# Kernel optimization log

Measured on AMD Instinct MI355X. Metric: run time of the kernel, lower is better.

The kernel has to match this reference:

```python
import jax, jax.numpy as jnp
import numpy as np

HIDDEN = 2048
QK_DIM = 2048
NUM_HEADS = 16
HEAD_DIM = QK_DIM // NUM_HEADS  # 128; RoPE rotates this many dims per head
B, T = 4, 2048
EPS = 1e-5


def setup_inputs() -> dict:
    key = jax.random.key(0)
    ks = jax.random.split(key, 10)
    return {
        "q_state": jax.random.normal(ks[0], (B, T, HIDDEN), jnp.float32),
        "k_state": jax.random.normal(ks[1], (B, T, HIDDEN), jnp.float32),
        "v_state": jax.random.normal(ks[2], (B, T, HIDDEN), jnp.float32),
        # torch Linear weights: [out_features, in_features], no bias
        "Wq": jax.random.normal(ks[3], (QK_DIM, HIDDEN), jnp.float32) * 0.02,
        "Wk": jax.random.normal(ks[4], (QK_DIM, HIDDEN), jnp.float32) * 0.02,
        "Wv": jax.random.normal(ks[5], (HIDDEN, HIDDEN), jnp.float32) * 0.02,
        "negator": jnp.asarray(1.0, jnp.float32),
        "q_gamma": jnp.ones((2 * QK_DIM,), jnp.float32),
        "q_beta": jnp.zeros((2 * QK_DIM,), jnp.float32),
        "k_gamma": jnp.ones((2 * QK_DIM,), jnp.float32),
        "k_beta": jnp.zeros((2 * QK_DIM,), jnp.float32),
        "offset": 0,
    }


def _layer_norm(x, gamma, beta):
    mu = jnp.mean(x, axis=-1, keepdims=True)
    var = jnp.mean(jnp.square(x - mu), axis=-1, keepdims=True)
    return (x - mu) * jax.lax.rsqrt(var + EPS) * gamma + beta


def _split_heads(x, n_heads):
    b, t, d = x.shape
    return x.reshape(b, t, n_heads, d // n_heads).transpose(0, 2, 1, 3)  # b h t f


def _rotate_half(x):
    # interleaved pairs: (x1, x2) -> (-x2, x1)
    x2 = x.reshape(*x.shape[:-1], x.shape[-1] // 2, 2)
    return jnp.stack((-x2[..., 1], x2[..., 0]), axis=-1).reshape(x.shape)


def _apply_rope(x, offset, rot_dim):
    # x: [b, h, t, f]; rotate first rot_dim features, pass the rest through
    t = (jnp.arange(x.shape[-2]) + offset).astype(jnp.float32)
    inv_freq = 1.0 / (10000.0 ** (jnp.arange(0, rot_dim, 2, dtype=jnp.float32) / rot_dim))
    freqs = t[:, None] * inv_freq[None, :]           # [t, rot_dim/2]
    freqs = jnp.repeat(freqs, 2, axis=-1)            # [t, rot_dim] interleaved
    cos, sin = jnp.cos(freqs), jnp.sin(freqs)
    xl, xr = x[..., :rot_dim], x[..., rot_dim:]
    xl = xl * cos + _rotate_half(xl) * sin
    return jnp.concatenate([xl, xr], axis=-1)


def reference(q_state, k_state, v_state, Wq, Wk, Wv, negator,
              q_gamma, q_beta, k_gamma, k_beta, offset):
    q = jnp.einsum("btd,fd->btf", q_state, Wq)
    k = jnp.einsum("btd,fd->btf", k_state, Wk)
    v = jnp.einsum("btd,fd->btf", v_state, Wv)
    q = jnp.concatenate((q, negator - q), axis=-1)   # [b, t, 2*QK_DIM]
    k = jnp.concatenate((k, negator - k), axis=-1)
    q = _layer_norm(q, q_gamma, q_beta)
    k = _layer_norm(k, k_gamma, k_beta)
    q = _split_heads(q, NUM_HEADS)                   # [b, h, t, 2*HEAD_DIM]
    k = _split_heads(k, NUM_HEADS)
    v = _split_heads(v, NUM_HEADS)                   # [b, h, t, HIDDEN/h]
    q = _apply_rope(q, offset, HEAD_DIM)
    k = _apply_rope(k, offset, HEAD_DIM)
    return q, k, v
```

## Files before the change

kernel.cpp:

```cpp
#include <hip/hip_runtime.h>
#include <hip/hip_fp16.h>

#define TDIM 2048
#define BDIM 4
#define MROWS 8192
#define NDIM 2048
#define KDIM 2048
#define NH 16

typedef __attribute__((ext_vector_type(8))) _Float16 f16x8;
typedef __attribute__((ext_vector_type(4))) _Float16 f16x4;
typedef __attribute__((ext_vector_type(4))) float f32x4;

__device__ __forceinline__ void load16_to_lds(const _Float16* g, _Float16* l) {
  __builtin_amdgcn_global_load_lds((const __attribute__((address_space(1))) void*)g,
                                   (__attribute__((address_space(3))) void*)l,
                                   16, 0, 0);
}

#define WAITBAR(N) do { \
  asm volatile("s_waitcnt vmcnt(" #N ")" ::: "memory"); \
  __builtin_amdgcn_s_barrier(); \
  __builtin_amdgcn_sched_barrier(0); \
} while (0)

__global__ __launch_bounds__(256) void cvt6_kernel(
    const float* __restrict__ s0, const float* __restrict__ s1,
    const float* __restrict__ s2, const float* __restrict__ s3,
    const float* __restrict__ s4, const float* __restrict__ s5,
    _Float16* __restrict__ d0, _Float16* __restrict__ d1,
    _Float16* __restrict__ d2, _Float16* __restrict__ d3,
    _Float16* __restrict__ d4, _Float16* __restrict__ d5) {
  const int z = blockIdx.z;
  const float* s; _Float16* d; int n;
  switch (z) {
    case 0: s = s0; d = d0; n = MROWS * KDIM; break;
    case 1: s = s1; d = d1; n = MROWS * KDIM; break;
    case 2: s = s2; d = d2; n = MROWS * KDIM; break;
    case 3: s = s3; d = d3; n = NDIM * KDIM; break;
    case 4: s = s4; d = d4; n = NDIM * KDIM; break;
    default: s = s5; d = d5; n = NDIM * KDIM; break;
  }
  const int n4 = n >> 2;
  const int stride = gridDim.x * blockDim.x;
  for (int i = blockIdx.x * blockDim.x + threadIdx.x; i < n4; i += stride) {
    float4 f = ((const float4*)s)[i];
    f16x4 h;
    h.x = (_Float16)f.x; h.y = (_Float16)f.y;
    h.z = (_Float16)f.z; h.w = (_Float16)f.w;
    ((f16x4*)d)[i] = h;
  }
}

__global__ __launch_bounds__(512, 2) void gemm_kernel(
    const _Float16* __restrict__ A0, const _Float16* __restrict__ A1,
    const _Float16* __restrict__ A2,
    const _Float16* __restrict__ W0, const _Float16* __restrict__ W1,
    const _Float16* __restrict__ W2,
    _Float16* __restrict__ qraw, _Float16* __restrict__ kraw,
    float* __restrict__ vout) {
  __shared__ __align__(16) _Float16 lds[4][2][8192];

  int lin = (blockIdx.z * gridDim.y + blockIdx.y) * gridDim.x + blockIdx.x;
  lin = (lin & 7) * 96 + (lin >> 3);
  const int z  = lin >> 8;
  const int ty = (lin >> 3) & 31;
  const int tx = lin & 7;

  const _Float16* __restrict__ A  = (z == 0) ? A0 : ((z == 1) ? A1 : A2);
  const _Float16* __restrict__ Wt = (z == 0) ? W0 : ((z == 1) ? W1 : W2);
  const int m0 = ty * 256;
  const int n0 = tx * 256;

  const int tid  = threadIdx.x;
  const int wave = tid >> 6;
  const int lane = tid & 63;
  const int m_in = lane & 15;
  const int kq   = lane >> 4;
  const int wave_m = wave >> 2;
  const int wave_n = wave & 3;

  f32x4 acc[8][4];
  const f32x4 z4 = {0.f, 0.f, 0.f, 0.f};
#pragma unroll
  for (int i = 0; i < 8; ++i)
#pragma unroll
    for (int j = 0; j < 4; ++j) acc[i][j] = z4;

  const int P0 = tid * 16;
  const int P1 = (512 + tid) * 16;
  const int L0 = P0 ^ (((P0 >> 7) & 3) << 4);
  const int L1 = P1 ^ (((P1 >> 7) & 3) << 4);
  const _Float16* srcA0 = A  + (size_t)(m0 + (L0 >> 6)) * KDIM + ((L0 & 63) >> 1);
  const _Float16* srcA1 = A  + (size_t)(m0 + (L1 >> 6)) * KDIM + ((L1 & 63) >> 1);
  const _Float16* srcB0 = Wt + (size_t)(n0 + (L0 >> 6)) * KDIM + ((L0 & 63) >> 1);
  const _Float16* srcB1 = Wt + (size_t)(n0 + (L1 >> 6)) * KDIM + ((L1 & 63) >> 1);
  const int dst0 = (wave * 64) * 8;
  const int dst1 = (512 + wave * 64) * 8;

  int offA[8], offB[4];
#pragma unroll
  for (int mi = 0; mi < 8; ++mi) {
    const int r = wave_m * 128 + mi * 16 + m_in;
    offA[mi] = r * 64 + ((kq ^ ((r >> 1) & 3)) << 4);
  }
#pragma unroll
  for (int ni = 0; ni < 4; ++ni) {
    const int r = wave_n * 64 + ni * 16 + m_in;
    offB[ni] = r * 64 + ((kq ^ ((r >> 1) & 3)) << 4);
  }

  auto stage = [&](int kt) {
    _Float16* base = &lds[kt & 3][0][0];
    const int ko = kt * 32;
    load16_to_lds(srcA0 + ko, base + dst0);
    load16_to_lds(srcA1 + ko, base + dst1);
    load16_to_lds(srcB0 + ko, base + 8192 + dst0);
    load16_to_lds(srcB1 + ko, base + 8192 + dst1);
  };

  auto compute = [&](int kt) {
    const char* Ab = (const char*)&lds[kt & 3][0][0];
    const char* Bb = (const char*)&lds[kt & 3][1][0];
    f16x8 a[8], b[4];
#pragma unroll
    for (int mi = 0; mi < 8; ++mi) a[mi] = *(const f16x8*)(Ab + offA[mi]);
#pragma unroll
    for (int ni = 0; ni < 4; ++ni) b[ni] = *(const f16x8*)(Bb + offB[ni]);
    __builtin_amdgcn_s_setprio(1);
#pragma unroll
    for (int mi = 0; mi < 8; ++mi)
#pragma unroll
      for (int ni = 0; ni < 4; ++ni)
        acc[mi][ni] = __builtin_amdgcn_mfma_f32_16x16x32_f16(a[mi], b[ni], acc[mi][ni], 0, 0, 0);
    __builtin_amdgcn_s_setprio(0);
  };

  stage(0); stage(1); stage(2);
  WAITBAR(8);

#pragma unroll 1
  for (int kt = 0; kt < KDIM / 32 - 3; ++kt) {
    stage(kt + 3);
    compute(kt);
    WAITBAR(8);
  }
  compute(KDIM / 32 - 3); WAITBAR(4);
  compute(KDIM / 32 - 2); WAITBAR(0);
  compute(KDIM / 32 - 1);

  const int rbase = kq * 4;
  const int wm = wave_m * 128;
  const int wn = wave_n * 64;
  if (z < 2) {
    _Float16* __restrict__ raw = (z == 0) ? qraw : kraw;
#pragma unroll
    for (int mi = 0; mi < 8; ++mi) {
      const int m = m0 + wm + mi * 16 + rbase;
#pragma unroll
      for (int ni = 0; ni < 4; ++ni) {
        const int n = n0 + wn + ni * 16 + m_in;
#pragma unroll
        for (int r = 0; r < 4; ++r)
          raw[(size_t)(m + r) * NDIM + n] = (_Float16)acc[mi][ni][r];
      }
    }
  } else {
#pragma unroll
    for (int mi = 0; mi < 8; ++mi) {
      const int mb = m0 + wm + mi * 16 + rbase;
#pragma unroll
      for (int ni = 0; ni < 4; ++ni) {
        const int n = n0 + wn + ni * 16 + m_in;
        const int h = n >> 7, dd = n & 127;
#pragma unroll
        for (int r = 0; r < 4; ++r) {
          const int m = mb + r;
          const int b = m >> 11, t = m & 2047;
          vout[(((size_t)(b * NH + h) * TDIM) + t) * 128 + dd] = acc[mi][ni][r];
        }
      }
    }
  }
}

__global__ __launch_bounds__(256) void ln_rope_kernel(
    const _Float16* __restrict__ qraw, const _Float16* __restrict__ kraw,
    const float* __restrict__ negator,
    const float* __restrict__ q_gamma, const float* __restrict__ q_beta,
    const float* __restrict__ k_gamma, const float* __restrict__ k_beta,
    const int* __restrict__ offset_p,
    float* __restrict__ out) {
  const int row = blockIdx.x;
  const int mat = blockIdx.y;
  const _Float16* __restrict__ raw = mat ? kraw : qraw;
  const float* __restrict__ gamma = mat ? k_gamma : q_gamma;
  const float* __restrict__ beta  = mat ? k_beta  : q_beta;
  float* __restrict__ outb = out + (size_t)mat * ((size_t)BDIM * NH * TDIM * 256);

  const float c = negator[0];
  const float mu = 0.5f * c;
  const int tid = threadIdx.x;

  __shared__ __align__(16) float vals[2048];
  __shared__ float wred[4];

  const int b = row >> 11, t = row & 2047;
  const float tpos = (float)(t + offset_p[0]);
  const int d = tid;

  float sv = 0.f, cv = 0.f;
  if (d < 128) {
    const int p = d >> 1;
    const float invf = exp2f(-(float)p * 0.20762050592854797f);
    sincosf(tpos * invf, &sv, &cv);
  }

  f16x8 hv = ((const f16x8*)(raw + (size_t)row * 2048))[tid];
  float v[8];
  float ss = 0.f;
#pragma unroll
  for (int j = 0; j < 8; ++j) {
    float x = (float)hv[j] - mu;
    v[j] = x;
    ss += x * x;
  }
  ((float4*)vals)[tid * 2 + 0] = make_float4(v[0], v[1], v[2], v[3]);
  ((float4*)vals)[tid * 2 + 1] = make_float4(v[4], v[5], v[6], v[7]);

#pragma unroll
  for (int o = 32; o > 0; o >>= 1) ss += __shfl_down(ss, o, 64);
  if ((tid & 63) == 0) wred[tid >> 6] = ss;
  __syncthreads();
  const float var = (wred[0] + wred[1] + wred[2] + wred[3]) * (1.0f / 2048.0f);
  const float rstd = rsqrtf(var + 1e-5f);

#pragma unroll
  for (int i = 0; i < 16; ++i) {
    const int g = i * 256 + tid;
    const float sgn = (g < 2048) ? 1.f : -1.f;
    const float y = sgn * vals[g & 2047] * rstd * gamma[g] + beta[g];
    float res;
    if (d < 128) {
      const int gp = g ^ 1;
      const float yp = sgn * vals[gp & 2047] * rstd * gamma[gp] + beta[gp];
      res = (d & 1) ? (y * cv + yp * sv) : (y * cv - yp * sv);
    } else {
      res = y;
    }
    outb[(((size_t)(b * NH + i) * TDIM) + t) * 256 + d] = res;
  }
}

extern "C" void kernel_launch(void* const* d_in, const int* in_sizes, int n_in,
                              void* d_out, int out_size, void* d_ws, size_t ws_size,
                              hipStream_t stream) {
  (void)in_sizes; (void)n_in; (void)out_size; (void)ws_size;
  const float* q_state = (const float*)d_in[0];
  const float* k_state = (const float*)d_in[1];
  const float* v_state = (const float*)d_in[2];
  const float* Wq = (const float*)d_in[3];
  const float* Wk = (const float*)d_in[4];
  const float* Wv = (const float*)d_in[5];
  const float* negator = (const float*)d_in[6];
  const float* q_gamma = (const float*)d_in[7];
  const float* q_beta  = (const float*)d_in[8];
  const float* k_gamma = (const float*)d_in[9];
  const float* k_beta  = (const float*)d_in[10];
  const int* offset    = (const int*)d_in[11];

  float* out = (float*)d_out;
  float* vout = out + (size_t)2 * BDIM * NH * TDIM * 256;

  _Float16* Aq   = (_Float16*)d_ws;
  _Float16* Ak   = Aq + (size_t)MROWS * KDIM;
  _Float16* Av   = Ak + (size_t)MROWS * KDIM;
  _Float16* Wq16 = Av + (size_t)MROWS * KDIM;
  _Float16* Wk16 = Wq16 + (size_t)NDIM * KDIM;
  _Float16* Wv16 = Wk16 + (size_t)NDIM * KDIM;
  _Float16* qraw = Wv16 + (size_t)NDIM * KDIM;
  _Float16* kraw = qraw + (size_t)MROWS * NDIM;

  cvt6_kernel<<<dim3(2048, 1, 6), dim3(256), 0, stream>>>(
      q_state, k_state, v_state, Wq, Wk, Wv, Aq, Ak, Av, Wq16, Wk16, Wv16);

  gemm_kernel<<<dim3(8, 32, 3), dim3(512), 0, stream>>>(
      Aq, Ak, Av, Wq16, Wk16, Wv16, qraw, kraw, vout);

  ln_rope_kernel<<<dim3(8192, 2), dim3(256), 0, stream>>>(
      qraw, kraw, negator, q_gamma, q_beta, k_gamma, k_beta, offset, out);
}
```

Baseline: 761.0 us.

## Vectorize cast and LN-RoPE stores, precompute RoPE sin/cos table

The fp32-to-fp16 cast now handles 8 elements per thread and writes 16-byte fp16 stores. A new small kernel precomputes a per-position cos/sin table into the no-longer-needed Wq16 workspace after the GEMM. The LN+RoPE kernel reads that table, and each thread processes 4 contiguous outputs with float4 loads and stores instead of scalar strided writes. This is meant to cut per-row sincos work and store transaction counts in the output-bandwidth-bound epilogue, at the cost of an extra launch and reliance on workspace reuse ordering.

Result: faster. 744.8 us (-2.1%).

```diff
diff --git a/kernel.cpp b/kernel.cpp
--- a/kernel.cpp
+++ b/kernel.cpp
@@ -41,15 +41,31 @@
     case 4: s = s4; d = d4; n = NDIM * KDIM; break;
     default: s = s5; d = d5; n = NDIM * KDIM; break;
   }
-  const int n4 = n >> 2;
+  const int n8 = n >> 3;
   const int stride = gridDim.x * blockDim.x;
-  for (int i = blockIdx.x * blockDim.x + threadIdx.x; i < n4; i += stride) {
-    float4 f = ((const float4*)s)[i];
-    f16x4 h;
-    h.x = (_Float16)f.x; h.y = (_Float16)f.y;
-    h.z = (_Float16)f.z; h.w = (_Float16)f.w;
-    ((f16x4*)d)[i] = h;
-  }
+  for (int i = blockIdx.x * blockDim.x + threadIdx.x; i < n8; i += stride) {
+    float4 f0 = ((const float4*)s)[i * 2 + 0];
+    float4 f1 = ((const float4*)s)[i * 2 + 1];
+    f16x8 h;
+    h[0] = (_Float16)f0.x; h[1] = (_Float16)f0.y;
+    h[2] = (_Float16)f0.z; h[3] = (_Float16)f0.w;
+    h[4] = (_Float16)f1.x; h[5] = (_Float16)f1.y;
+    h[6] = (_Float16)f1.z; h[7] = (_Float16)f1.w;
+    ((f16x8*)d)[i] = h;
+  }
+}
+
+__global__ __launch_bounds__(256) void rope_fill_kernel(
+    const int* __restrict__ offset_p, float* __restrict__ tab) {
+  const int idx = blockIdx.x * blockDim.x + threadIdx.x;
+  if (idx >= TDIM * 64) return;
+  const int t = idx >> 6, p = idx & 63;
+  const float tpos = (float)(t + offset_p[0]);
+  const float invf = exp2f(-(float)p * 0.20762050592854797f);
+  float sv, cv;
+  sincosf(tpos * invf, &sv, &cv);
+  tab[idx * 2 + 0] = cv;
+  tab[idx * 2 + 1] = sv;
 }
 
 __global__ __launch_bounds__(512, 2) void gemm_kernel(
@@ -189,7 +205,7 @@
     const float* __restrict__ negator,
     const float* __restrict__ q_gamma, const float* __restrict__ q_beta,
     const float* __restrict__ k_gamma, const float* __restrict__ k_beta,
-    const int* __restrict__ offset_p,
+    const float* __restrict__ rope_tab,
     float* __restrict__ out) {
   const int row = blockIdx.x;
   const int mat = blockIdx.y;
@@ -206,15 +222,6 @@
   __shared__ float wred[4];
 
   const int b = row >> 11, t = row & 2047;
-  const float tpos = (float)(t + offset_p[0]);
-  const int d = tid;
-
-  float sv = 0.f, cv = 0.f;
-  if (d < 128) {
-    const int p = d >> 1;
-    const float invf = exp2f(-(float)p * 0.20762050592854797f);
-    sincosf(tpos * invf, &sv, &cv);
-  }
 
   f16x8 hv = ((const f16x8*)(raw + (size_t)row * 2048))[tid];
   float v[8];
@@ -235,20 +242,33 @@
   const float var = (wred[0] + wred[1] + wred[2] + wred[3]) * (1.0f / 2048.0f);
   const float rstd = rsqrtf(var + 1e-5f);
 
-#pragma unroll
-  for (int i = 0; i < 16; ++i) {
-    const int g = i * 256 + tid;
-    const float sgn = (g < 2048) ? 1.f : -1.f;
-    const float y = sgn * vals[g & 2047] * rstd * gamma[g] + beta[g];
-    float res;
-    if (d < 128) {
-      const int gp = g ^ 1;
-      const float yp = sgn * vals[gp & 2047] * rstd * gamma[gp] + beta[gp];
-      res = (d & 1) ? (y * cv + yp * sv) : (y * cv - yp * sv);
+  const float4* __restrict__ tab4 = (const float4*)(rope_tab + (size_t)t * 128);
+
+#pragma unroll
+  for (int j = 0; j < 4; ++j) {
+    const int g0 = j * 1024 + tid * 4;
+    const float sgn = (g0 < 2048) ? 1.f : -1.f;
+    const float4 val = ((const float4*)vals)[(g0 & 2047) >> 2];
+    const float4 gm  = ((const float4*)gamma)[g0 >> 2];
+    const float4 bt  = ((const float4*)beta)[g0 >> 2];
+    float y0 = sgn * val.x * rstd * gm.x + bt.x;
+    float y1 = sgn * val.y * rstd * gm.y + bt.y;
+    float y2 = sgn * val.z * rstd * gm.z + bt.z;
+    float y3 = sgn * val.w * rstd * gm.w + bt.w;
+
+    const int h  = g0 >> 8;
+    const int d0 = g0 & 255;
+    float4 res;
+    if (d0 < 128) {
+      const float4 cs = tab4[d0 >> 2];
+      res.x = y0 * cs.x - y1 * cs.y;
+      res.y = y1 * cs.x + y0 * cs.y;
+      res.z = y2 * cs.z - y3 * cs.w;
+      res.w = y3 * cs.z + y2 * cs.w;
     } else {
-      res = y;
+      res = make_float4(y0, y1, y2, y3);
     }
-    outb[(((size_t)(b * NH + i) * TDIM) + t) * 256 + d] = res;
+    ((float4*)(outb + (((size_t)(b * NH + h) * TDIM) + t) * 256))[d0 >> 2] = res;
   }
 }
 
@@ -281,12 +301,16 @@
   _Float16* qraw = Wv16 + (size_t)NDIM * KDIM;
   _Float16* kraw = qraw + (size_t)MROWS * NDIM;
 
+  float* rope_tab = (float*)Wq16;
+
   cvt6_kernel<<<dim3(2048, 1, 6), dim3(256), 0, stream>>>(
       q_state, k_state, v_state, Wq, Wk, Wv, Aq, Ak, Av, Wq16, Wk16, Wv16);
 
   gemm_kernel<<<dim3(8, 32, 3), dim3(512), 0, stream>>>(
       Aq, Ak, Av, Wq16, Wk16, Wv16, qraw, kraw, vout);
 
+  rope_fill_kernel<<<dim3(512), dim3(256), 0, stream>>>(offset, rope_tab);
+
   ln_rope_kernel<<<dim3(8192, 2), dim3(256), 0, stream>>>(
-      qraw, kraw, negator, q_gamma, q_beta, k_gamma, k_beta, offset, out);
-}
+      qraw, kraw, negator, q_gamma, q_beta, k_gamma, k_beta, rope_tab, out);
+}
```
